# Optimization experiments

Hardware: AMD Instinct MI355X
Metric: run time of the kernel (lower is better)

## Reference

```python
import jax, jax.numpy as jnp
import numpy as np

IN_CH_IMG = 256
CHANNELS = 256
NUM_CLASSES = 1
NUM_LAYERS = 4  # NUM_FC=3 -> 4 layers
IN_CH = IN_CH_IMG + 256  # pos-enc adds 256 channels
N_INST = 128
N_PTS = 2048

W_SIZES = [IN_CH * CHANNELS, CHANNELS * CHANNELS, CHANNELS * CHANNELS, CHANNELS * NUM_CLASSES]
B_SIZES = [CHANNELS, CHANNELS, CHANNELS, NUM_CLASSES]
NUM_PARAMS = sum(W_SIZES) + sum(B_SIZES)  # 263169


def setup_inputs() -> dict:
    key = jax.random.key(0)
    k1, k2, k3, k4 = jax.random.split(key, 4)
    return {
        "fine_grained_features": jax.random.normal(k1, (N_INST, IN_CH_IMG, N_PTS), dtype=jnp.float32),
        "point_coords": jax.random.uniform(k2, (N_INST, N_PTS, 2), dtype=jnp.float32),
        "parameters": jax.random.normal(k3, (N_INST, NUM_PARAMS), dtype=jnp.float32) * 0.05,
        "pe_gaussian": jax.random.normal(k4, (2, 128), dtype=jnp.float32),
    }


def _parse_params(params):
    # params: [N, NUM_PARAMS]. Weight blocks first, then bias blocks.
    n = params.shape[0]
    out_dims = [CHANNELS, CHANNELS, CHANNELS, NUM_CLASSES]
    in_dims = [IN_CH, CHANNELS, CHANNELS, CHANNELS]
    weights, biases = [], []
    off = 0
    for l in range(NUM_LAYERS):
        weights.append(params[:, off:off + W_SIZES[l]].reshape(n, out_dims[l], in_dims[l]))
        off += W_SIZES[l]
    for l in range(NUM_LAYERS):
        biases.append(params[:, off:off + B_SIZES[l]].reshape(n, out_dims[l], 1))
        off += B_SIZES[l]
    return weights, biases


def reference(fine_grained_features, point_coords, parameters, pe_gaussian):
    n, _, p = fine_grained_features.shape
    # Positional encoding: [N*P, 2] -> [N*P, 128] -> sin/cos -> [N, 256, P]
    loc = (2.0 * point_coords.reshape(n * p, 2) - 1.0) @ pe_gaussian
    loc = 2.0 * np.pi * loc
    pe = jnp.concatenate([jnp.sin(loc), jnp.cos(loc)], axis=1)  # [N*P, 256]
    pe = pe.reshape(n, p, 256).transpose(0, 2, 1)  # [N, 256, P]
    x = jnp.concatenate([pe, fine_grained_features], axis=1)  # [N, IN_CH, P]

    weights, biases = _parse_params(parameters)
    for i, (w, b) in enumerate(zip(weights, biases)):
        x = jnp.einsum('nck,ndc->ndk', x, w) + b
        if i < NUM_LAYERS - 1:
            x = jax.nn.relu(x)
    return x.reshape(-1, NUM_CLASSES, p)  # [N, 1, P]
```

## Files before the change

kernel.cpp:

```cpp
#include <hip/hip_runtime.h>
#include <hip/hip_fp16.h>


#define NI      128
#define NPTS    2048
#define CH      256
#define NPARAM  263169
#define PT      64
#define NTILES  (NPTS / PT)
#define ROWS    536

#define WOFF0   0
#define WOFF1   131072
#define WOFF2   196608
#define WOFF3   262144
#define BOFF0   262400
#define BOFF1   262656
#define BOFF2   262912
#define BOFF3   263168

#define PI_L0   0
#define PI_L1   131072
#define PI_L2   196608
#define PI_L3   262144
#define WS_PER_INST 262400
#define WS_BYTES ((size_t)NI * WS_PER_INST * 2)

typedef _Float16 f16x8 __attribute__((ext_vector_type(8)));
typedef float    f32x4 __attribute__((ext_vector_type(4)));

__global__ __launch_bounds__(256) void iph_prep(
    const float* __restrict__ params, _Float16* __restrict__ wsw)
{
    const int inst = blockIdx.y;
    const int r = blockIdx.x * 256 + threadIdx.x;
    if (r >= 32800) return;
    const float* __restrict__ P = params + (size_t)inst * NPARAM;
    _Float16* __restrict__ W = wsw + (size_t)inst * WS_PER_INST;

    int rl, woff, K, dst;
    if (r < 16384)      { rl = r;         woff = WOFF0; K = 512; dst = PI_L0; }
    else if (r < 24576) { rl = r - 16384; woff = WOFF1; K = 256; dst = PI_L1; }
    else if (r < 32768) { rl = r - 24576; woff = WOFF2; K = 256; dst = PI_L2; }
    else {
        const int e = (r - 32768) * 8;
        f16x8 v;
        #pragma unroll
        for (int j = 0; j < 8; ++j) v[j] = (_Float16)P[WOFF3 + e + j];
        *(f16x8*)&W[PI_L3 + e] = v;
        return;
    }
    const int e    = rl * 8;
    const int lane = rl & 63;
    const int cb   = (rl >> 6) & 15;
    const int ks   = rl >> 10;
    const int co   = cb * 16 + (lane & 15);
    const int k    = ks * 32 + (lane >> 4) * 8;
    const float* __restrict__ src = P + woff + co * K + k;
    f16x8 v;
    #pragma unroll
    for (int j = 0; j < 8; ++j) v[j] = (_Float16)src[j];
    *(f16x8*)&W[dst + e] = v;
}

template<bool PREPPED>
__global__ __launch_bounds__(512, 4) void iph_main(
    const float* __restrict__ feat,
    const float* __restrict__ coords,
    const float* __restrict__ params,
    const _Float16* __restrict__ wsw,
    const float* __restrict__ peg,
    float* __restrict__ out)
{
    __shared__ _Float16 X[PT * ROWS];

    const int bid  = blockIdx.x;
    const int inst = (bid & 7) | ((bid >> 8) << 3);
    const int tile = (bid >> 3) & 31;
    const int p0   = tile * PT;
    const int tid  = threadIdx.x;
    const float* __restrict__ P = params + (size_t)inst * NPARAM;
    const _Float16* __restrict__ WI = wsw + (size_t)inst * WS_PER_INST;

    {
        const int pt   = tid >> 3;
        const int part = tid & 7;
        const float cx = coords[((size_t)inst * NPTS + p0 + pt) * 2 + 0];
        const float cy = coords[((size_t)inst * NPTS + p0 + pt) * 2 + 1];
        const float a = 2.f * cx - 1.f;
        const float b = 2.f * cy - 1.f;
        #pragma unroll
        for (int j = 0; j < 16; ++j) {
            const int f = part * 16 + j;
            float locr = a * peg[f] + b * peg[128 + f];
            locr -= floorf(locr);
            const float s = __builtin_amdgcn_sinf(locr);
            const float c = __builtin_amdgcn_cosf(locr);
            X[pt * ROWS + f]       = (_Float16)s;
            X[pt * ROWS + 128 + f] = (_Float16)c;
        }
    }
    {
        #pragma unroll 4
        for (int it = 0; it < 32; ++it) {
            const int idx = it * 512 + tid;
            const int c = idx >> 6;
            const int p = idx & 63;
            const float v = feat[((size_t)inst * CH + c) * NPTS + p0 + p];
            X[p * ROWS + 256 + c] = (_Float16)v;
        }
    }
    __syncthreads();

    const int lane = tid & 63;
    const int wave = tid >> 6;
    const int l15  = lane & 15;
    const int hi   = lane >> 4;

    auto run_layer = [&](const int foff, const int woff, const int boff, const int K) {
        f32x4 acc[4][2];
        #pragma unroll
        for (int mt = 0; mt < 4; ++mt)
            #pragma unroll
            for (int nt = 0; nt < 2; ++nt)
                acc[mt][nt] = (f32x4){0.f, 0.f, 0.f, 0.f};

        const int nks = K >> 5;
        for (int ks = 0; ks < nks; ++ks) {
            f16x8 bfrag[2];
            #pragma unroll
            for (int nt = 0; nt < 2; ++nt) {
                if (PREPPED) {
                    const int cb = wave * 2 + nt;
                    bfrag[nt] = *(const f16x8*)&WI[foff + (((ks * 16 + cb) * 64 + lane) << 3)];
                } else {
                    const int co = wave * 32 + nt * 16 + l15;
                    const float* wp = P + woff + (size_t)co * K + ks * 32 + hi * 8;
                    float w8[8];
                    __builtin_memcpy(w8, wp, 32);
                    f16x8 bb;
                    #pragma unroll
                    for (int j = 0; j < 8; ++j) bb[j] = (_Float16)w8[j];
                    bfrag[nt] = bb;
                }
            }
            f16x8 afrag[4];
            #pragma unroll
            for (int mt = 0; mt < 4; ++mt) {
                const int pt = mt * 16 + l15;
                afrag[mt] = *(const f16x8*)&X[pt * ROWS + ks * 32 + hi * 8];
            }
            #pragma unroll
            for (int mt = 0; mt < 4; ++mt)
                #pragma unroll
                for (int nt = 0; nt < 2; ++nt)
                    acc[mt][nt] = __builtin_amdgcn_mfma_f32_16x16x32_f16(
                        afrag[mt], bfrag[nt], acc[mt][nt], 0, 0, 0);
        }

        float bias[2];
        #pragma unroll
        for (int nt = 0; nt < 2; ++nt)
            bias[nt] = P[boff + wave * 32 + nt * 16 + l15];

        __syncthreads();
        #pragma unroll
        for (int mt = 0; mt < 4; ++mt) {
            #pragma unroll
            for (int nt = 0; nt < 2; ++nt) {
                #pragma unroll
                for (int r = 0; r < 4; ++r) {
                    float v = acc[mt][nt][r] + bias[nt];
                    v = fmaxf(v, 0.f);
                    const int pt = mt * 16 + hi * 4 + r;
                    const int ch = wave * 32 + nt * 16 + l15;
                    X[pt * ROWS + ch] = (_Float16)v;
                }
            }
        }
        __syncthreads();
    };

    run_layer(PI_L0, WOFF0, BOFF0, 512);
    run_layer(PI_L1, WOFF1, BOFF1, 256);
    run_layer(PI_L2, WOFF2, BOFF2, 256);

    if (tid < PT) {
        const int pt = tid;
        float sum = P[BOFF3];
        const f16x8* row = (const f16x8*)&X[pt * ROWS];
        if (PREPPED) {
            #pragma unroll 8
            for (int j = 0; j < 32; ++j) {
                const f16x8 v = row[j];
                const f16x8 w = *(const f16x8*)&WI[PI_L3 + j * 8];
                #pragma unroll
                for (int q = 0; q < 8; ++q) sum += (float)v[q] * (float)w[q];
            }
        } else {
            #pragma unroll 8
            for (int j = 0; j < 32; ++j) {
                const f16x8 v = row[j];
                const float* wp = P + WOFF3 + j * 8;
                float w8[8];
                __builtin_memcpy(w8, wp, 32);
                #pragma unroll
                for (int q = 0; q < 8; ++q) sum += (float)v[q] * w8[q];
            }
        }
        out[(size_t)inst * NPTS + p0 + pt] = sum;
    }
}

extern "C" void kernel_launch(void* const* d_in, const int* in_sizes, int n_in,
                              void* d_out, int out_size, void* d_ws, size_t ws_size,
                              hipStream_t stream) {
    (void)in_sizes; (void)n_in; (void)out_size;
    const float* feat   = (const float*)d_in[0];
    const float* coords = (const float*)d_in[1];
    const float* params = (const float*)d_in[2];
    const float* peg    = (const float*)d_in[3];
    float* out = (float*)d_out;

    dim3 grid(NI * NTILES);
    dim3 block(512);

    if (ws_size >= WS_BYTES) {
        _Float16* wsw = (_Float16*)d_ws;
        iph_prep<<<dim3(129, 128), dim3(256), 0, stream>>>(params, wsw);
        iph_main<true><<<grid, block, 0, stream>>>(feat, coords, params, wsw, peg, out);
    } else {
        iph_main<false><<<grid, block, 0, stream>>>(feat, coords, params,
                                                    (const _Float16*)d_ws, peg, out);
    }
}
```

Before: 259.6 us.

## Vectorize LDS stores with packed fp16 conversion and parallelize final layer

Weight output-channel mapping is interleaved so each lane owns two adjacent output channels, letting the epilogue write packed half2 values to LDS instead of scalar halves. The positional-encoding and feature staging now convert with cvt_pkrtz and store 16-byte vectors, reducing LDS store count. The last 256->1 layer is spread across all 512 threads with shuffle reduction instead of 64 threads looping serially. The K loop gets unroll 2. Round-toward-zero conversion slightly changes numerics versus round-to-nearest.

```diff
diff --git a/kernel.cpp b/kernel.cpp
--- a/kernel.cpp
+++ b/kernel.cpp
@@ -26,8 +26,11 @@
 #define WS_PER_INST 262400
 #define WS_BYTES ((size_t)NI * WS_PER_INST * 2)
 
+typedef __fp16   h16x2 __attribute__((ext_vector_type(2)));
 typedef _Float16 f16x8 __attribute__((ext_vector_type(8)));
 typedef float    f32x4 __attribute__((ext_vector_type(4)));
+
+union pack8 { h16x2 h[4]; f16x8 v; };
 
 __global__ __launch_bounds__(256) void iph_prep(
     const float* __restrict__ params, _Float16* __restrict__ wsw)
@@ -54,7 +57,7 @@
     const int lane = rl & 63;
     const int cb   = (rl >> 6) & 15;
     const int ks   = rl >> 10;
-    const int co   = cb * 16 + (lane & 15);
+    const int co   = (cb >> 1) * 32 + 2 * (lane & 15) + (cb & 1);
     const int k    = ks * 32 + (lane >> 4) * 8;
     const float* __restrict__ src = P + woff + co * K + k;
     f16x8 v;
@@ -79,43 +82,59 @@
     const int tile = (bid >> 3) & 31;
     const int p0   = tile * PT;
     const int tid  = threadIdx.x;
+    const int lane = tid & 63;
+    const int wave = tid >> 6;
+    const int l15  = lane & 15;
+    const int hi   = lane >> 4;
     const float* __restrict__ P = params + (size_t)inst * NPARAM;
     const _Float16* __restrict__ WI = wsw + (size_t)inst * WS_PER_INST;
 
     {
         const int pt   = tid >> 3;
         const int part = tid & 7;
-        const float cx = coords[((size_t)inst * NPTS + p0 + pt) * 2 + 0];
-        const float cy = coords[((size_t)inst * NPTS + p0 + pt) * 2 + 1];
-        const float a = 2.f * cx - 1.f;
-        const float b = 2.f * cy - 1.f;
+        const float2 cc = *(const float2*)&coords[((size_t)inst * NPTS + p0 + pt) * 2];
+        const float a = 2.f * cc.x - 1.f;
+        const float b = 2.f * cc.y - 1.f;
+        float sv[16], cv[16];
         #pragma unroll
         for (int j = 0; j < 16; ++j) {
             const int f = part * 16 + j;
             float locr = a * peg[f] + b * peg[128 + f];
             locr -= floorf(locr);
-            const float s = __builtin_amdgcn_sinf(locr);
-            const float c = __builtin_amdgcn_cosf(locr);
-            X[pt * ROWS + f]       = (_Float16)s;
-            X[pt * ROWS + 128 + f] = (_Float16)c;
-        }
+            sv[j] = __builtin_amdgcn_sinf(locr);
+            cv[j] = __builtin_amdgcn_cosf(locr);
+        }
+        pack8 s0, s1, c0, c1;
+        #pragma unroll
+        for (int q = 0; q < 4; ++q) {
+            s0.h[q] = __builtin_amdgcn_cvt_pkrtz(sv[2*q],     sv[2*q + 1]);
+            s1.h[q] = __builtin_amdgcn_cvt_pkrtz(sv[8 + 2*q], sv[9 + 2*q]);
+            c0.h[q] = __builtin_amdgcn_cvt_pkrtz(cv[2*q],     cv[2*q + 1]);
+            c1.h[q] = __builtin_amdgcn_cvt_pkrtz(cv[8 + 2*q], cv[9 + 2*q]);
+        }
+        _Float16* base = &X[pt * ROWS + part * 16];
+        *(f16x8*)(base)           = s0.v;
+        *(f16x8*)(base + 8)       = s1.v;
+        *(f16x8*)(base + 128)     = c0.v;
+        *(f16x8*)(base + 136)     = c1.v;
     }
     {
-        #pragma unroll 4
-        for (int it = 0; it < 32; ++it) {
-            const int idx = it * 512 + tid;
-            const int c = idx >> 6;
-            const int p = idx & 63;
-            const float v = feat[((size_t)inst * CH + c) * NPTS + p0 + p];
-            X[p * ROWS + 256 + c] = (_Float16)v;
+        const float* fbase = feat + (size_t)inst * CH * NPTS + p0 + lane;
+        #pragma unroll
+        for (int s = 0; s < 4; ++s) {
+            const int c0i = s * 64 + wave * 8;
+            float w8[8];
+            #pragma unroll
+            for (int j = 0; j < 8; ++j)
+                w8[j] = fbase[(size_t)(c0i + j) * NPTS];
+            pack8 pk;
+            #pragma unroll
+            for (int q = 0; q < 4; ++q)
+                pk.h[q] = __builtin_amdgcn_cvt_pkrtz(w8[2*q], w8[2*q + 1]);
+            *(f16x8*)&X[lane * ROWS + 256 + c0i] = pk.v;
         }
     }
     __syncthreads();
-
-    const int lane = tid & 63;
-    const int wave = tid >> 6;
-    const int l15  = lane & 15;
-    const int hi   = lane >> 4;
 
     auto run_layer = [&](const int foff, const int woff, const int boff, const int K) {
         f32x4 acc[4][2];
@@ -126,6 +145,7 @@
                 acc[mt][nt] = (f32x4){0.f, 0.f, 0.f, 0.f};
 
         const int nks = K >> 5;
+        #pragma unroll 2
         for (int ks = 0; ks < nks; ++ks) {
             f16x8 bfrag[2];
             #pragma unroll
@@ -134,7 +154,7 @@
                     const int cb = wave * 2 + nt;
                     bfrag[nt] = *(const f16x8*)&WI[foff + (((ks * 16 + cb) * 64 + lane) << 3)];
                 } else {
-                    const int co = wave * 32 + nt * 16 + l15;
+                    const int co = wave * 32 + 2 * l15 + nt;
                     const float* wp = P + woff + (size_t)co * K + ks * 32 + hi * 8;
                     float w8[8];
                     __builtin_memcpy(w8, wp, 32);
@@ -146,10 +166,8 @@
             }
             f16x8 afrag[4];
             #pragma unroll
-            for (int mt = 0; mt < 4; ++mt) {
-                const int pt = mt * 16 + l15;
-                afrag[mt] = *(const f16x8*)&X[pt * ROWS + ks * 32 + hi * 8];
-            }
+            for (int mt = 0; mt < 4; ++mt)
+                afrag[mt] = *(const f16x8*)&X[(mt * 16 + l15) * ROWS + ks * 32 + hi * 8];
             #pragma unroll
             for (int mt = 0; mt < 4; ++mt)
                 #pragma unroll
@@ -158,24 +176,18 @@
                         afrag[mt], bfrag[nt], acc[mt][nt], 0, 0, 0);
         }
 
-        float bias[2];
-        #pragma unroll
-        for (int nt = 0; nt < 2; ++nt)
-            bias[nt] = P[boff + wave * 32 + nt * 16 + l15];
+        const float2 bb = *(const float2*)&P[boff + wave * 32 + 2 * l15];
 
         __syncthreads();
         #pragma unroll
         for (int mt = 0; mt < 4; ++mt) {
             #pragma unroll
-            for (int nt = 0; nt < 2; ++nt) {
-                #pragma unroll
-                for (int r = 0; r < 4; ++r) {
-                    float v = acc[mt][nt][r] + bias[nt];
-                    v = fmaxf(v, 0.f);
-                    const int pt = mt * 16 + hi * 4 + r;
-                    const int ch = wave * 32 + nt * 16 + l15;
-                    X[pt * ROWS + ch] = (_Float16)v;
-                }
+            for (int r = 0; r < 4; ++r) {
+                const float v0 = fmaxf(acc[mt][0][r] + bb.x, 0.f);
+                const float v1 = fmaxf(acc[mt][1][r] + bb.y, 0.f);
+                const h16x2 e = __builtin_amdgcn_cvt_pkrtz(v0, v1);
+                const int pt = mt * 16 + hi * 4 + r;
+                *(h16x2*)&X[pt * ROWS + wave * 32 + 2 * l15] = e;
             }
         }
         __syncthreads();
@@ -185,30 +197,30 @@
     run_layer(PI_L1, WOFF1, BOFF1, 256);
     run_layer(PI_L2, WOFF2, BOFF2, 256);
 
-    if (tid < PT) {
-        const int pt = tid;
-        float sum = P[BOFF3];
-        const f16x8* row = (const f16x8*)&X[pt * ROWS];
-        if (PREPPED) {
-            #pragma unroll 8
-            for (int j = 0; j < 32; ++j) {
-                const f16x8 v = row[j];
-                const f16x8 w = *(const f16x8*)&WI[PI_L3 + j * 8];
+    {
+        const int pt   = tid >> 3;
+        const int part = tid & 7;
+        float sum = 0.f;
+        #pragma unroll
+        for (int q = 0; q < 4; ++q) {
+            const f16x8 v = *(const f16x8*)&X[pt * ROWS + part * 8 + q * 64];
+            if (PREPPED) {
+                const f16x8 w = *(const f16x8*)&WI[PI_L3 + part * 8 + q * 64];
                 #pragma unroll
-                for (int q = 0; q < 8; ++q) sum += (float)v[q] * (float)w[q];
-            }
-        } else {
-            #pragma unroll 8
-            for (int j = 0; j < 32; ++j) {
-                const f16x8 v = row[j];
-                const float* wp = P + WOFF3 + j * 8;
+                for (int j = 0; j < 8; ++j) sum += (float)v[j] * (float)w[j];
+            } else {
+                const float* wp = P + WOFF3 + part * 8 + q * 64;
                 float w8[8];
                 __builtin_memcpy(w8, wp, 32);
                 #pragma unroll
-                for (int q = 0; q < 8; ++q) sum += (float)v[q] * w8[q];
+                for (int j = 0; j < 8; ++j) sum += (float)v[j] * w8[j];
             }
         }
-        out[(size_t)inst * NPTS + p0 + pt] = sum;
+        sum += __shfl_xor(sum, 1);
+        sum += __shfl_xor(sum, 2);
+        sum += __shfl_xor(sum, 4);
+        if (part == 0)
+            out[(size_t)inst * NPTS + p0 + pt] = sum + P[BOFF3];
     }
 }
 
```

Measured after the change: 242.9 us. 6.4% less time.
